# Kernel optimization log

Measured on AMD Instinct MI355X. Metric: run time of the kernel, lower is better.

## Reference

```python
import jax, jax.numpy as jnp
import numpy as np
import math

B, T, C, H = 2, 2048, 1024, 16
HD = C // H  # head_dim = 64
SCALE = 1.0 / math.sqrt(HD)


def _e8_head_dirs(n_heads: int) -> np.ndarray:
    # Type-1 E8 roots in original generation order: (+-1 at i, +-1 at j), i<j,
    # sign order (-1,-1),(-1,1),(1,-1),(1,1); then L2-normalized (norm sqrt(2)).
    roots = []
    for i in range(8):
        for j in range(i + 1, 8):
            for si in (-1.0, 1.0):
                for sj in (-1.0, 1.0):
                    r = np.zeros(8, dtype=np.float32)
                    r[i] = si
                    r[j] = sj
                    roots.append(r)
    roots = np.stack(roots)  # [112, 8], first n_heads used
    roots = roots / np.linalg.norm(roots, axis=1, keepdims=True)
    return roots[:n_heads]


def setup_inputs() -> dict:
    key = jax.random.key(0)
    k1, k2, k3, k4 = jax.random.split(key, 4)
    x = jax.random.normal(k1, (B, T, C), dtype=jnp.float32)
    # nn.Linear-style init scale
    w_qkv = jax.random.normal(k2, (C, 3 * C), dtype=jnp.float32) * (1.0 / math.sqrt(C))
    w_out = jax.random.normal(k3, (C, C), dtype=jnp.float32) * (1.0 / math.sqrt(C))
    head_scales = jax.random.normal(k4, (H,), dtype=jnp.float32) * 0.1
    head_dirs = jnp.asarray(_e8_head_dirs(H))  # [H, 8] buffer (not trained)
    return {"x": x, "w_qkv": w_qkv, "w_out": w_out,
            "head_scales": head_scales, "head_dirs": head_dirs}


def reference(x, w_qkv, w_out, head_scales, head_dirs):
    Bx, Tx, Cx = x.shape
    qkv = (x @ w_qkv).reshape(Bx, Tx, 3, H, HD)
    qkv = jnp.transpose(qkv, (2, 0, 3, 1, 4))  # [3, B, H, T, HD]
    q, k, v = qkv[0], qkv[1], qkv[2]
    scores = jnp.einsum('bhqd,bhkd->bhqk', q, k) * SCALE  # [B,H,T,T]
    causal = jnp.tril(jnp.ones((Tx, Tx), dtype=bool))
    scores = jnp.where(causal[None, None], scores, -jnp.inf)
    # E8 geometric bias: rank-1 per-head bias from projections onto root dirs
    q_proj = jnp.einsum('bhtd,hd->bht', q[..., :8], head_dirs)
    k_proj = jnp.einsum('bhtd,hd->bht', k[..., :8], head_dirs)
    geo_bias = q_proj[..., :, None] * k_proj[..., None, :]  # [B,H,T,T]
    scores = scores + head_scales[None, :, None, None] * geo_bias
    attn = jax.nn.softmax(scores, axis=-1)
    out = jnp.einsum('bhqk,bhkd->bhqd', attn, v)  # [B,H,T,HD]
    out = jnp.transpose(out, (0, 2, 1, 3)).reshape(Bx, Tx, Cx)
    return out @ w_out
```

## Files before the change

kernel.cpp:

```cpp
#include <hip/hip_runtime.h>
#include <stdint.h>


typedef float f32x4 __attribute__((ext_vector_type(4)));
typedef unsigned short u16x8 __attribute__((ext_vector_type(8)));
typedef unsigned short u16x4 __attribute__((ext_vector_type(4)));
typedef unsigned int u32x2 __attribute__((ext_vector_type(2)));
typedef __bf16 bf16x8 __attribute__((ext_vector_type(8)));

static __device__ __forceinline__ unsigned short f2bf(float f) {
  unsigned u = __float_as_uint(f);
  u += 0x7FFFu + ((u >> 16) & 1u);
  return (unsigned short)(u >> 16);
}
static __device__ __forceinline__ float bf2f(unsigned short s) {
  return __uint_as_float(((unsigned)s) << 16);
}
static __device__ __forceinline__ f32x4 mfma16(u16x8 a, u16x8 b, f32x4 c) {
  return __builtin_amdgcn_mfma_f32_16x16x32_bf16(
      __builtin_bit_cast(bf16x8, a), __builtin_bit_cast(bf16x8, b), c, 0, 0, 0);
}
static __device__ __forceinline__ unsigned cvtpk(float lo, float hi) {
  unsigned d;
  asm("v_cvt_pk_bf16_f32 %0, %1, %2" : "=v"(d) : "v"(lo), "v"(hi));
  return d;
}

#define GLD16(gp, lp) __builtin_amdgcn_global_load_lds( \
    (const __attribute__((address_space(1))) unsigned int*)(gp), \
    (__attribute__((address_space(3))) unsigned int*)(lp), 16, 0, 0)

__global__ __launch_bounds__(256) void k_prep(const float* __restrict__ x,
                                              const float* __restrict__ wqkv,
                                              const float* __restrict__ wout,
                                              unsigned short* __restrict__ xb,
                                              unsigned short* __restrict__ wqkvT,
                                              unsigned short* __restrict__ woutT) {
  __shared__ float t[64][65];
  const int bid = blockIdx.x;
  if (bid < 4096) {
    int i = bid * 256 + threadIdx.x;
    f32x4 v = *(const f32x4*)(x + (size_t)i * 4);
    u16x4 o;
#pragma unroll
    for (int j = 0; j < 4; ++j) o[j] = f2bf(v[j]);
    *(u16x4*)(xb + (size_t)i * 4) = o;
    return;
  }
  const float* in;
  unsigned short* out;
  int Cc, bx, by;
  if (bid < 4864) {
    int tt = bid - 4096;
    in = wqkv; out = wqkvT; Cc = 3072;
    bx = tt % 48; by = tt / 48;
  } else {
    int tt = bid - 4864;
    in = wout; out = woutT; Cc = 1024;
    bx = tt & 15; by = tt >> 4;
  }
  const int R = 1024;
  int tr = by * 64, tc = bx * 64;
  int tx = threadIdx.x & 15, ty = threadIdx.x >> 4;
#pragma unroll
  for (int i = 0; i < 4; ++i) {
    int rr = ty + i * 16;
    f32x4 v = *(const f32x4*)(in + (size_t)(tr + rr) * Cc + tc + tx * 4);
#pragma unroll
    for (int j = 0; j < 4; ++j) t[rr][tx * 4 + j] = v[j];
  }
  __syncthreads();
#pragma unroll
  for (int i = 0; i < 4; ++i) {
    int cc = ty + i * 16;
    int rr = tx * 4;
    u16x4 o;
#pragma unroll
    for (int j = 0; j < 4; ++j) o[j] = f2bf(t[rr + j][cc]);
    *(u16x4*)(out + (size_t)(tc + cc) * R + tr + rr) = o;
  }
}

template <int MODE>
__global__ __launch_bounds__(256) void k_gemm(const unsigned short* __restrict__ A,
                                              const unsigned short* __restrict__ Bt,
                                              unsigned short* __restrict__ qo,
                                              unsigned short* __restrict__ ko,
                                              unsigned short* __restrict__ vTo,
                                              float* __restrict__ fo) {
  __shared__ unsigned short lA[128 * 32];
  __shared__ unsigned short lB[128 * 32];
  const int tid = threadIdx.x;
  const int lane = tid & 63, wid = tid >> 6;
  const int wr = wid >> 1, wc = wid & 1;
  const int r = lane & 15, g = lane >> 4;
  const int mbase = blockIdx.y * 128;
  const int nbase = blockIdx.x * 128;

  f32x4 acc[4][4] = {};

  for (int kt = 0; kt < 32; ++kt) {
    __syncthreads();
#pragma unroll
    for (int p = 0; p < 2; ++p) {
      int L = p * 4096 + tid * 16;
      int row = L >> 6;
      int blk = (L >> 4) & 3;
      GLD16(A + (size_t)(mbase + row) * 1024 + kt * 32 + blk * 8, lA + (L >> 1));
      GLD16(Bt + (size_t)(nbase + row) * 1024 + kt * 32 + blk * 8, lB + (L >> 1));
    }
    __syncthreads();
    u16x8 af[4], bfv[4];
#pragma unroll
    for (int m = 0; m < 4; ++m)
      af[m] = *(const u16x8*)(lA + (wr * 64 + m * 16 + r) * 32 + g * 8);
#pragma unroll
    for (int n = 0; n < 4; ++n)
      bfv[n] = *(const u16x8*)(lB + (wc * 64 + n * 16 + r) * 32 + g * 8);
#pragma unroll
    for (int m = 0; m < 4; ++m)
#pragma unroll
      for (int n = 0; n < 4; ++n) acc[m][n] = mfma16(af[m], bfv[n], acc[m][n]);
  }

#pragma unroll
  for (int m = 0; m < 4; ++m) {
#pragma unroll
    for (int n = 0; n < 4; ++n) {
      int ng = nbase + wc * 64 + n * 16 + r;
      int m0 = mbase + wr * 64 + m * 16 + g * 4;
      if (MODE == 0) {
        int sec = ng >> 10, rem = ng & 1023, hh = rem >> 6, d = rem & 63;
        int b = m0 >> 11, t0 = m0 & 2047;
        size_t bh = (size_t)(b * 16 + hh);
        if (sec == 2) {
          u16x4 o;
#pragma unroll
          for (int e = 0; e < 4; ++e) o[e] = f2bf(acc[m][n][e]);
          *(u16x4*)(vTo + (bh * 64 + d) * 2048 + t0) = o;
        } else {
          unsigned short* dst = (sec == 0 ? qo : ko);
#pragma unroll
          for (int e = 0; e < 4; ++e)
            dst[(bh * 2048 + t0 + e) * 64 + d] = f2bf(acc[m][n][e]);
        }
      } else {
#pragma unroll
        for (int e = 0; e < 4; ++e)
          fo[(size_t)(m0 + e) * 1024 + ng] = acc[m][n][e];
      }
    }
  }
}

__global__ __launch_bounds__(256) void k_attn(const unsigned short* __restrict__ qb,
                                              const unsigned short* __restrict__ kb,
                                              const unsigned short* __restrict__ vTb,
                                              const float* __restrict__ hsc,
                                              const float* __restrict__ hdir,
                                              unsigned short* __restrict__ o2) {
  __shared__ unsigned short lK[2][64 * 64];
  __shared__ unsigned short lV[2][64 * 64];
  __shared__ unsigned short lP[4][16 * 64];

  const int tid = threadIdx.x, lane = tid & 63, wid = tid >> 6;
  const int r = lane & 15, g = lane >> 4;
  const int bid = blockIdx.x;
  const int u = bid & 255, kq = bid >> 8;
  const int bh = u & 31, j = u >> 5;
  const int a = (kq == 0) ? j : (kq == 1) ? (31 - j) : (kq == 2) ? (8 + j) : (23 - j);
  const int nk = a + 1;
  const int qbase = a * 64;
  const int h = bh & 15, bi = bh >> 4;

  const size_t kbase = (size_t)bh * (2048 * 64);
  const size_t vbase = (size_t)bh * (64 * 2048);

  auto STAGE = [&](int buf, int kt) {
    unsigned short* dK = (unsigned short*)lK[buf];
    unsigned short* dV = (unsigned short*)lV[buf];
#pragma unroll
    for (int p = 0; p < 2; ++p) {
      int L = p * 4096 + tid * 16;
      int row = L >> 7;
      int cb = (L >> 4) & 7;
      int cbg = cb ^ (row & 7);
      GLD16(kb + kbase + (size_t)(kt * 64 + row) * 64 + cbg * 8, dK + (L >> 1));
      GLD16(vTb + vbase + (size_t)row * 2048 + kt * 64 + cbg * 8, dV + (L >> 1));
    }
  };

  STAGE(0, 0);

  const float LOG2E = 1.44269504088896f;
  const float hs = hsc[h];
  float dir8[8];
#pragma unroll
  for (int j2 = 0; j2 < 8; ++j2) dir8[j2] = hdir[h * 8 + j2];

  u16x8 qc0, qc1;
  {
    const unsigned short* qrow = qb + ((size_t)bh * 2048 + qbase + wid * 16 + r) * 64;
    float proj = 0.f;
    u16x8 qv = *(const u16x8*)qrow;
#pragma unroll
    for (int j2 = 0; j2 < 8; ++j2) proj += bf2f(qv[j2]) * dir8[j2];
#pragma unroll
    for (int s = 0; s < 2; ++s) {
      u16x8 raw = *(const u16x8*)(qrow + s * 32 + g * 8);
      u16x8 ov;
#pragma unroll
      for (int j2 = 0; j2 < 8; ++j2) {
        float v = bf2f(raw[j2]) * (0.125f * LOG2E);
        if (s == 0 && g == 0) v += (hs * LOG2E) * proj * dir8[j2];
        ov[j2] = f2bf(v);
      }
      if (s == 0) qc0 = ov; else qc1 = ov;
    }
  }

  f32x4 accO[4] = {};
  float lp = 0.f;
  unsigned short* pw = &lP[wid][0];
  const int swz = (r & 7) << 4;
  const int qq = qbase + wid * 16 + r;

  for (int kt = 0; kt < nk; ++kt) {
    asm volatile("s_waitcnt lgkmcnt(0)" ::: "memory");
    __builtin_amdgcn_sched_barrier(0);
    __builtin_amdgcn_s_barrier();
    __builtin_amdgcn_sched_barrier(0);

    if (kt + 1 < nk) STAGE((kt + 1) & 1, kt + 1);

    if (kt + 1 < nk) {
      asm volatile("s_waitcnt vmcnt(4)" ::: "memory");
    } else {
      asm volatile("s_waitcnt vmcnt(0)" ::: "memory");
    }
    __builtin_amdgcn_sched_barrier(0);
    __builtin_amdgcn_s_barrier();
    __builtin_amdgcn_sched_barrier(0);

    const char* lKc = (const char*)lK[kt & 1];
    const char* lVc = (const char*)lV[kt & 1];

    f32x4 accS[4];
    __builtin_amdgcn_s_setprio(1);
#pragma unroll
    for (int ct = 0; ct < 4; ++ct) {
      f32x4 s4 = {0.f, 0.f, 0.f, 0.f};
      int krow = ct * 16 + r;
      int sw = (krow & 7) << 4;
      u16x8 kf0 = *(const u16x8*)(lKc + krow * 128 + ((g * 16) ^ sw));
      u16x8 kf1 = *(const u16x8*)(lKc + krow * 128 + ((64 + g * 16) ^ sw));
      s4 = mfma16(kf0, qc0, s4);
      s4 = mfma16(kf1, qc1, s4);
      accS[ct] = s4;
    }
    __builtin_amdgcn_s_setprio(0);

    if (kt == nk - 1) {
#pragma unroll
      for (int ct = 0; ct < 4; ++ct)
#pragma unroll
        for (int e = 0; e < 4; ++e) {
          int kk = kt * 64 + ct * 16 + g * 4 + e;
          if (kk > qq) accS[ct][e] = -1e30f;
        }
    }

    float p[4][4];
#pragma unroll
    for (int ct = 0; ct < 4; ++ct)
#pragma unroll
      for (int e = 0; e < 4; ++e) p[ct][e] = exp2f(accS[ct][e]);
#pragma unroll
    for (int ct = 0; ct < 4; ++ct)
      lp += (p[ct][0] + p[ct][1]) + (p[ct][2] + p[ct][3]);

#pragma unroll
    for (int ct = 0; ct < 4; ++ct) {
      u32x2 w;
      w[0] = cvtpk(p[ct][0], p[ct][1]);
      w[1] = cvtpk(p[ct][2], p[ct][3]);
      *(u32x2*)((char*)pw + r * 128 + ((ct * 32 + g * 8) ^ swz)) = w;
    }
    asm volatile("s_waitcnt lgkmcnt(0)" ::: "memory");
    __builtin_amdgcn_sched_barrier(0);

    __builtin_amdgcn_s_setprio(1);
#pragma unroll
    for (int s = 0; s < 2; ++s) {
      u16x8 pa = *(const u16x8*)((const char*)pw + r * 128 + ((s * 64 + g * 16) ^ swz));
#pragma unroll
      for (int dt = 0; dt < 4; ++dt) {
        int dd = dt * 16 + r;
        u16x8 vf = *(const u16x8*)(lVc + dd * 128 + ((s * 64 + g * 16) ^ ((dd & 7) << 4)));
        accO[dt] = mfma16(vf, pa, accO[dt]);
      }
    }
    __builtin_amdgcn_s_setprio(0);
  }

  lp += __shfl_xor(lp, 16, 64);
  lp += __shfl_xor(lp, 32, 64);
  float inv = 1.f / lp;
#pragma unroll
  for (int dt = 0; dt < 4; ++dt) {
    u16x4 o;
#pragma unroll
    for (int e = 0; e < 4; ++e) o[e] = f2bf(accO[dt][e] * inv);
    *(u16x4*)(o2 + ((size_t)(bi * 2048 + qq)) * 1024 + h * 64 + dt * 16 + g * 4) = o;
  }
}

extern "C" void kernel_launch(void* const* d_in, const int* in_sizes, int n_in,
                              void* d_out, int out_size, void* d_ws, size_t ws_size,
                              hipStream_t stream) {
  const float* x    = (const float*)d_in[0];
  const float* wqkv = (const float*)d_in[1];
  const float* wout = (const float*)d_in[2];
  const float* hsc  = (const float*)d_in[3];
  const float* hdir = (const float*)d_in[4];
  float* outp = (float*)d_out;

  char* ws = (char*)d_ws;
  unsigned short* xb    = (unsigned short*)(ws + 0);
  unsigned short* wqkvT = (unsigned short*)(ws + 8388608);
  unsigned short* woutT = (unsigned short*)(ws + 14680064);
  unsigned short* qb    = (unsigned short*)(ws + 16777216);
  unsigned short* kb    = (unsigned short*)(ws + 25165824);
  unsigned short* vT    = (unsigned short*)(ws + 33554432);
  unsigned short* x2b   = (unsigned short*)(ws + 41943040);
  if (ws_size < 50331648u) return;

  k_prep<<<5120, 256, 0, stream>>>(x, wqkv, wout, xb, wqkvT, woutT);
  k_gemm<0><<<dim3(24, 32), 256, 0, stream>>>(xb, wqkvT, qb, kb, vT, nullptr);
  k_attn<<<dim3(1024), 256, 0, stream>>>(qb, kb, vT, hsc, hdir, x2b);
  k_gemm<1><<<dim3(8, 32), 256, 0, stream>>>(x2b, woutT, nullptr, nullptr, nullptr, outp);
}
```

Before: 111.9 us.

## Rewrite QKV GEMM with 256x256 tiles and a 4-stage async LDS pipeline

Replaces the templated QKV projection GEMM with a dedicated kernel that uses 512 threads, 256x256 output tiles, and a 4-deep LDS ring buffer. Global loads are issued three k-steps ahead and split across two half-steps, with explicit waitcnt, barriers and setprio so loads overlap the MFMA work. A swizzled block index is added for L2 locality. The out-projection GEMM keeps the old single-buffered design. The larger tiles cut the QKV launch from 768 blocks to 192, which on a 256-CU part leaves some CUs idle and may expose the pipeline to ordering or synchronisation mistakes.

```diff
diff --git a/kernel.cpp b/kernel.cpp
--- a/kernel.cpp
+++ b/kernel.cpp
@@ -81,13 +81,124 @@
   }
 }
 
-template <int MODE>
-__global__ __launch_bounds__(256) void k_gemm(const unsigned short* __restrict__ A,
-                                              const unsigned short* __restrict__ Bt,
-                                              unsigned short* __restrict__ qo,
-                                              unsigned short* __restrict__ ko,
-                                              unsigned short* __restrict__ vTo,
-                                              float* __restrict__ fo) {
+__global__ __launch_bounds__(512, 1) void k_gemm_qkv(const unsigned short* __restrict__ A,
+                                                     const unsigned short* __restrict__ Bt,
+                                                     unsigned short* __restrict__ qo,
+                                                     unsigned short* __restrict__ ko,
+                                                     unsigned short* __restrict__ vTo) {
+  __shared__ unsigned short lA[4][256 * 32];
+  __shared__ unsigned short lB[4][256 * 32];
+  const int tid = threadIdx.x;
+  const int lane = tid & 63, wid = tid >> 6;
+  const int wr = wid >> 2, wc = wid & 3;
+  const int r = lane & 15, g = lane >> 4;
+  const int bid0 = blockIdx.x;
+  const int swz = (bid0 & 7) * 24 + (bid0 >> 3);
+  const int mbase = (swz / 12) * 256, nbase = (swz % 12) * 256;
+
+  auto STAGE_A = [&](int buf, int kt) {
+#pragma unroll
+    for (int p = 0; p < 2; ++p) {
+      int L = p * 8192 + tid * 16;
+      int row = L >> 6, cb = (L >> 4) & 3;
+      GLD16(A + (size_t)(mbase + row) * 1024 + kt * 32 + cb * 8, lA[buf] + (L >> 1));
+    }
+  };
+  auto STAGE_B = [&](int buf, int kt) {
+#pragma unroll
+    for (int p = 0; p < 2; ++p) {
+      int L = p * 8192 + tid * 16;
+      int row = L >> 6, cb = (L >> 4) & 3;
+      GLD16(Bt + (size_t)(nbase + row) * 1024 + kt * 32 + cb * 8, lB[buf] + (L >> 1));
+    }
+  };
+
+  f32x4 acc[8][4] = {};
+
+  STAGE_A(0, 0); STAGE_B(0, 0);
+  STAGE_A(1, 1); STAGE_B(1, 1);
+  STAGE_A(2, 2); STAGE_B(2, 2);
+  asm volatile("s_waitcnt vmcnt(8)" ::: "memory");
+  __builtin_amdgcn_sched_barrier(0);
+  __builtin_amdgcn_s_barrier();
+
+  for (int t = 0; t < 32; ++t) {
+    const int buf = t & 3;
+    const int nbuf = (t + 3) & 3;
+    const unsigned short* pA = lA[buf];
+    const unsigned short* pB = lB[buf];
+
+    u16x8 bf[4], af[4];
+#pragma unroll
+    for (int nf = 0; nf < 4; ++nf)
+      bf[nf] = *(const u16x8*)(pB + (wc * 64 + nf * 16 + r) * 32 + g * 8);
+#pragma unroll
+    for (int mf = 0; mf < 4; ++mf)
+      af[mf] = *(const u16x8*)(pA + (wr * 128 + mf * 16 + r) * 32 + g * 8);
+    if (t + 3 < 32) STAGE_A(nbuf, t + 3);
+    __builtin_amdgcn_s_barrier();
+    asm volatile("s_waitcnt lgkmcnt(0)" ::: "memory");
+    __builtin_amdgcn_sched_barrier(0);
+    __builtin_amdgcn_s_setprio(1);
+#pragma unroll
+    for (int mf = 0; mf < 4; ++mf)
+#pragma unroll
+      for (int nf = 0; nf < 4; ++nf) acc[mf][nf] = mfma16(af[mf], bf[nf], acc[mf][nf]);
+    __builtin_amdgcn_s_setprio(0);
+    __builtin_amdgcn_s_barrier();
+
+#pragma unroll
+    for (int mf = 0; mf < 4; ++mf)
+      af[mf] = *(const u16x8*)(pA + (wr * 128 + (mf + 4) * 16 + r) * 32 + g * 8);
+    if (t + 3 < 32) STAGE_B(nbuf, t + 3);
+    __builtin_amdgcn_s_barrier();
+    asm volatile("s_waitcnt lgkmcnt(0)" ::: "memory");
+    __builtin_amdgcn_sched_barrier(0);
+    __builtin_amdgcn_s_setprio(1);
+#pragma unroll
+    for (int mf = 0; mf < 4; ++mf)
+#pragma unroll
+      for (int nf = 0; nf < 4; ++nf) acc[mf + 4][nf] = mfma16(af[mf], bf[nf], acc[mf + 4][nf]);
+    __builtin_amdgcn_s_setprio(0);
+
+    if (t < 29) {
+      asm volatile("s_waitcnt vmcnt(8)" ::: "memory");
+    } else if (t == 29) {
+      asm volatile("s_waitcnt vmcnt(4)" ::: "memory");
+    } else if (t == 30) {
+      asm volatile("s_waitcnt vmcnt(0)" ::: "memory");
+    }
+    __builtin_amdgcn_sched_barrier(0);
+    __builtin_amdgcn_s_barrier();
+  }
+
+#pragma unroll
+  for (int mf = 0; mf < 8; ++mf) {
+#pragma unroll
+    for (int nf = 0; nf < 4; ++nf) {
+      int ng = nbase + wc * 64 + nf * 16 + r;
+      int m0 = mbase + wr * 128 + mf * 16 + g * 4;
+      int sec = ng >> 10, rem = ng & 1023, hh = rem >> 6, d = rem & 63;
+      int b = m0 >> 11, t0 = m0 & 2047;
+      size_t bh = (size_t)(b * 16 + hh);
+      if (sec == 2) {
+        u16x4 o;
+#pragma unroll
+        for (int e = 0; e < 4; ++e) o[e] = f2bf(acc[mf][nf][e]);
+        *(u16x4*)(vTo + (bh * 64 + d) * 2048 + t0) = o;
+      } else {
+        unsigned short* dst = (sec == 0 ? qo : ko);
+#pragma unroll
+        for (int e = 0; e < 4; ++e)
+          dst[(bh * 2048 + t0 + e) * 64 + d] = f2bf(acc[mf][nf][e]);
+      }
+    }
+  }
+}
+
+__global__ __launch_bounds__(256) void k_gemm_out(const unsigned short* __restrict__ A,
+                                                  const unsigned short* __restrict__ Bt,
+                                                  float* __restrict__ fo) {
   __shared__ unsigned short lA[128 * 32];
   __shared__ unsigned short lB[128 * 32];
   const int tid = threadIdx.x;
@@ -124,33 +235,15 @@
   }
 
 #pragma unroll
-  for (int m = 0; m < 4; ++m) {
+  for (int m = 0; m < 4; ++m)
 #pragma unroll
     for (int n = 0; n < 4; ++n) {
       int ng = nbase + wc * 64 + n * 16 + r;
       int m0 = mbase + wr * 64 + m * 16 + g * 4;
-      if (MODE == 0) {
-        int sec = ng >> 10, rem = ng & 1023, hh = rem >> 6, d = rem & 63;
-        int b = m0 >> 11, t0 = m0 & 2047;
-        size_t bh = (size_t)(b * 16 + hh);
-        if (sec == 2) {
-          u16x4 o;
-#pragma unroll
-          for (int e = 0; e < 4; ++e) o[e] = f2bf(acc[m][n][e]);
-          *(u16x4*)(vTo + (bh * 64 + d) * 2048 + t0) = o;
-        } else {
-          unsigned short* dst = (sec == 0 ? qo : ko);
-#pragma unroll
-          for (int e = 0; e < 4; ++e)
-            dst[(bh * 2048 + t0 + e) * 64 + d] = f2bf(acc[m][n][e]);
-        }
-      } else {
-#pragma unroll
-        for (int e = 0; e < 4; ++e)
-          fo[(size_t)(m0 + e) * 1024 + ng] = acc[m][n][e];
-      }
-    }
-  }
+#pragma unroll
+      for (int e = 0; e < 4; ++e)
+        fo[(size_t)(m0 + e) * 1024 + ng] = acc[m][n][e];
+    }
 }
 
 __global__ __launch_bounds__(256) void k_attn(const unsigned short* __restrict__ qb,
@@ -336,7 +429,7 @@
   if (ws_size < 50331648u) return;
 
   k_prep<<<5120, 256, 0, stream>>>(x, wqkv, wout, xb, wqkvT, woutT);
-  k_gemm<0><<<dim3(24, 32), 256, 0, stream>>>(xb, wqkvT, qb, kb, vT, nullptr);
+  k_gemm_qkv<<<192, 512, 0, stream>>>(xb, wqkvT, qb, kb, vT);
   k_attn<<<dim3(1024), 256, 0, stream>>>(qb, kb, vT, hsc, hdir, x2b);
-  k_gemm<1><<<dim3(8, 32), 256, 0, stream>>>(x2b, woutT, nullptr, nullptr, nullptr, outp);
-}
+  k_gemm_out<<<dim3(8, 32), 256, 0, stream>>>(x2b, woutT, outp);
+}
```

Measured after the change: 118.3 us. 5.7% more time.
